# Performance work log

Hardware: AMD Instinct MI355X
Metric: run time of the kernel (lower is better)

The kernel has to match this reference:

```python
import jax, jax.numpy as jnp
import numpy as np

H, W, C_IN, C_ADD = 721, 1440, 78, 8
N_NODES, K = 5882, 128
DAY_OF_YEAR = 182.5  # module default time_of_year
LN_EPS = 1e-5        # haiku LayerNorm default
NORM_EPS = 1e-7


def setup_inputs() -> dict:
    key = jax.random.key(0)
    ks = jax.random.split(key, 4)
    return {
        "var_grid": jax.random.normal(ks[0], (H, W, C_IN), dtype=jnp.float32),
        "nearby_idx": jax.random.randint(ks[1], (N_NODES, K), 0, H * W),
        "input_means": jnp.zeros((C_IN + C_ADD,), jnp.float32),
        "input_stds": jnp.ones((C_IN + C_ADD,), jnp.float32),
        "W1": jax.random.normal(ks[2], (C_IN + C_ADD, 256), dtype=jnp.float32) * 0.1,
        "b1": jnp.zeros((256,), jnp.float32),
        "ln_scale": jnp.ones((256,), jnp.float32),
        "ln_offset": jnp.zeros((256,), jnp.float32),
        "W2": jax.random.normal(ks[3], (256, 256), dtype=jnp.float32) * 0.1,
        "b2": jnp.zeros((256,), jnp.float32),
    }


def _additional_features(h, w):
    # 8 extra channels: sin/cos of lat/lon, normalized day-of-year, 3 zero pads
    lat = jnp.linspace(-90.0, 90.0, h)
    lon = jnp.linspace(0.0, 360.0, w)
    lat2d = jnp.broadcast_to(lat[:, None], (h, w))
    lon2d = jnp.broadcast_to(lon[None, :], (h, w))
    lat_r, lon_r = jnp.radians(lat2d), jnp.radians(lon2d)
    day = jnp.float32(DAY_OF_YEAR / 365.0)
    z = jnp.zeros((h, w), jnp.float32)
    return jnp.stack([
        jnp.sin(lat_r), jnp.cos(lat_r), jnp.sin(lon_r), jnp.cos(lon_r),
        jnp.full((h, w), day, jnp.float32), z, z, z,
    ], axis=-1)  # [H, W, 8]


def reference(var_grid, nearby_idx, input_means, input_stds,
              W1, b1, ln_scale, ln_offset, W2, b2):
    h, w, c = var_grid.shape
    add = _additional_features(h, w)                       # [H, W, 8]
    flat = jnp.concatenate([var_grid, add], -1).reshape(h * w, c + C_ADD)
    gathered = flat[nearby_idx]                            # [N, K, 86] irregular gather
    x = (gathered - input_means) / (input_stds + NORM_EPS)
    hidden = jax.nn.relu(jnp.einsum('nkc,cd->nkd', x, W1) + b1)
    mu = hidden.mean(-1, keepdims=True)
    var = hidden.var(-1, keepdims=True)
    hidden = (hidden - mu) * jax.lax.rsqrt(var + LN_EPS) * ln_scale + ln_offset
    nodes = jnp.einsum('nkd,de->nke', hidden, W2) + b2     # [N, K, 256]
    return nodes
```

## Files before the change

### kernel.cpp

```cpp
#include <hip/hip_runtime.h>
#include <hip/hip_bf16.h>
#include <math.h>

#define GH 721
#define GW 1440
#define C_IN 78
#define NNODES 5882
#define KNEIGH 128
#define M_TOTAL (NNODES * KNEIGH)
#define TM 32
#define NBLOCKS (M_TOTAL / TM)

typedef __attribute__((ext_vector_type(8))) short bf16x8;
typedef __attribute__((ext_vector_type(4))) float f32x4;

__device__ __forceinline__ unsigned short f2bf(float x) {
    __hip_bfloat16 b = __float2bfloat16(x);
    union { __hip_bfloat16 h; unsigned short u; } cv; cv.h = b; return cv.u;
}

__global__ void prep_kernel(const float* __restrict__ W1, const float* __restrict__ W2,
                            const float* __restrict__ means, const float* __restrict__ stds,
                            const float* __restrict__ b1, const float* __restrict__ lnS,
                            const float* __restrict__ lnO, const float* __restrict__ b2,
                            unsigned short* __restrict__ bp1, unsigned short* __restrict__ bp2,
                            float* __restrict__ latT, float* __restrict__ lonT,
                            float* __restrict__ b1p, float* __restrict__ K1,
                            float* __restrict__ K2)
{
    const int NB1 = 3 * 4 * 256 * 8;
    const int NB2 = 8 * 4 * 256 * 8;
    const int NTOT = NB1 + NB2 + GH + GW + 256;
    for (int e = blockIdx.x * blockDim.x + threadIdx.x; e < NTOT;
         e += gridDim.x * blockDim.x) {
        if (e < NB1) {
            int j = e & 7, c = (e >> 3) & 255, o = (e >> 11) & 3, s = e >> 13;
            int k = s * 32 + o * 8 + j;
            float v = 0.f;
            if (k < 82) v = W1[k * 256 + c] / (stds[k] + 1e-7f);
            bp1[e] = f2bf(v);
        } else if (e < NB1 + NB2) {
            int t = e - NB1;
            int j = t & 7, c = (t >> 3) & 255, o = (t >> 11) & 3, s = t >> 13;
            int k = s * 32 + o * 8 + j;
            bp2[t] = f2bf(W2[k * 256 + c] * lnS[k]);
        } else if (e < NB1 + NB2 + GH) {
            int h = e - NB1 - NB2;
            float r = (-90.f + 0.25f * (float)h) * 0.017453292519943295f;
            latT[2 * h]     = sinf(r);
            latT[2 * h + 1] = cosf(r);
        } else if (e < NB1 + NB2 + GH + GW) {
            int w = e - NB1 - NB2 - GH;
            float r = ((float)w * (360.f / 1439.f)) * 0.017453292519943295f;
            lonT[2 * w]     = sinf(r);
            lonT[2 * w + 1] = cosf(r);
        } else {
            int c = e - NB1 - NB2 - GH - GW;
            float acc = b1[c];
            #pragma unroll 1
            for (int k = 0; k < 86; ++k) {
                float inv = 1.f / (stds[k] + 1e-7f);
                float w = W1[k * 256 + c] * inv;
                acc -= means[k] * w;
                if (k == 82) acc += 0.5f * w;
            }
            b1p[c] = acc;
            float k1 = 0.f, k2 = 0.f;
            #pragma unroll 1
            for (int k = 0; k < 256; ++k) {
                float w = W2[k * 256 + c];
                k1 += lnS[k] * w;
                k2 += lnO[k] * w;
            }
            K1[c] = k1;
            K2[c] = k2 + b2[c];
        }
    }
}

__global__ __launch_bounds__(256, 4)
void fused_kernel(const float* __restrict__ var_grid, const int* __restrict__ idxs,
                  const unsigned short* __restrict__ bp1, const unsigned short* __restrict__ bp2,
                  const float* __restrict__ latT, const float* __restrict__ lonT,
                  const float* __restrict__ b1p, const float* __restrict__ K1,
                  const float* __restrict__ K2,
                  float* __restrict__ out)
{
    __shared__ __align__(16) unsigned short x_lds[TM][104];
    __shared__ __align__(16) unsigned short h_lds[TM * 256];
    __shared__ float red[2][4][TM];

    const int swz = (blockIdx.x & 7) * 2941 + (blockIdx.x >> 3);

    const int tid  = threadIdx.x;
    const int lane = tid & 63;
    const int wc   = tid >> 6;
    const int l15  = lane & 15;
    const int lg   = lane >> 4;
    const int wbase = wc * 64;
    const long block0 = (long)swz * TM;

    {
        const int row = tid >> 3, p = tid & 7;
        const int idx = idxs[block0 + row];
        const int hh = idx / GW;
        const int ww = idx - hh * GW;
        const float* src = var_grid + (long)idx * C_IN;
        float2 g[5], tl, tl2;
        #pragma unroll
        for (int t = 0; t < 5; ++t) {
            const int q = p + 8 * t;
            if (q < 39) g[t] = *(const float2*)(src + 2 * q);
        }
        tl.x  = latT[2 * hh]; tl.y  = latT[2 * hh + 1];
        tl2.x = lonT[2 * ww]; tl2.y = lonT[2 * ww + 1];
        unsigned int* xrow = (unsigned int*)&x_lds[row][0];
        #pragma unroll
        for (int t = 0; t < 6; ++t) {
            const int q = p + 8 * t;
            float v0, v1;
            if (q < 39)      { v0 = g[t].x; v1 = g[t].y; }
            else if (q == 39){ v0 = tl.x;  v1 = tl.y; }
            else if (q == 40){ v0 = tl2.x; v1 = tl2.y; }
            else             { v0 = 0.f; v1 = 0.f; }
            xrow[q] = ((unsigned int)f2bf(v1) << 16) | (unsigned int)f2bf(v0);
        }
    }

    float b1v[4];
    #pragma unroll
    for (int nf = 0; nf < 4; ++nf) b1v[nf] = b1p[wbase + nf * 16 + l15];
    __syncthreads();

    f32x4 acc[2][4];
    #pragma unroll
    for (int mf = 0; mf < 2; ++mf)
        #pragma unroll
        for (int nf = 0; nf < 4; ++nf) acc[mf][nf] = (f32x4){0.f, 0.f, 0.f, 0.f};

    #pragma unroll
    for (int s = 0; s < 3; ++s) {
        bf16x8 af[2], bw[4];
        #pragma unroll
        for (int nf = 0; nf < 4; ++nf)
            bw[nf] = *(const bf16x8*)(bp1 + ((size_t)((s * 4 + lg) * 256) + wbase + nf * 16 + l15) * 8);
        #pragma unroll
        for (int mf = 0; mf < 2; ++mf)
            af[mf] = *(const bf16x8*)&x_lds[mf * 16 + l15][s * 32 + lg * 8];
        #pragma unroll
        for (int mf = 0; mf < 2; ++mf)
            #pragma unroll
            for (int nf = 0; nf < 4; ++nf)
                acc[mf][nf] = __builtin_amdgcn_mfma_f32_16x16x32_bf16(af[mf], bw[nf], acc[mf][nf], 0, 0, 0);
    }

    float sm[2][4], sq[2][4];
    #pragma unroll
    for (int mf = 0; mf < 2; ++mf)
        #pragma unroll
        for (int i = 0; i < 4; ++i) { sm[mf][i] = 0.f; sq[mf][i] = 0.f; }

    #pragma unroll
    for (int mf = 0; mf < 2; ++mf)
        #pragma unroll
        for (int nf = 0; nf < 4; ++nf)
            #pragma unroll
            for (int i = 0; i < 4; ++i) {
                float v = fmaxf(acc[mf][nf][i] + b1v[nf], 0.f);
                sm[mf][i] += v;
                sq[mf][i] += v * v;
                int row = mf * 16 + lg * 4 + i;
                int col = wbase + nf * 16 + l15;
                unsigned off = (unsigned)(row * 512 + col * 2);
                off ^= (unsigned)((row & 7) << 4);
                *(unsigned short*)((char*)h_lds + off) = f2bf(v);
            }

    #pragma unroll
    for (int m = 1; m < 16; m <<= 1)
        #pragma unroll
        for (int mf = 0; mf < 2; ++mf)
            #pragma unroll
            for (int i = 0; i < 4; ++i) {
                sm[mf][i] += __shfl_xor(sm[mf][i], m, 64);
                sq[mf][i] += __shfl_xor(sq[mf][i], m, 64);
            }

    if (l15 == 0) {
        #pragma unroll
        for (int mf = 0; mf < 2; ++mf)
            #pragma unroll
            for (int i = 0; i < 4; ++i) {
                int row = mf * 16 + lg * 4 + i;
                red[0][wc][row] = sm[mf][i];
                red[1][wc][row] = sq[mf][i];
            }
    }
    __syncthreads();

    #pragma unroll
    for (int mf = 0; mf < 2; ++mf)
        #pragma unroll
        for (int nf = 0; nf < 4; ++nf) acc[mf][nf] = (f32x4){0.f, 0.f, 0.f, 0.f};

    #pragma unroll
    for (int s = 0; s < 8; ++s) {
        bf16x8 af[2], bw[4];
        #pragma unroll
        for (int nf = 0; nf < 4; ++nf)
            bw[nf] = *(const bf16x8*)(bp2 + ((size_t)((s * 4 + lg) * 256) + wbase + nf * 16 + l15) * 8);
        #pragma unroll
        for (int mf = 0; mf < 2; ++mf) {
            int row = mf * 16 + l15;
            unsigned off = (unsigned)(row * 512 + (s * 32 + lg * 8) * 2);
            off ^= (unsigned)((row & 7) << 4);
            af[mf] = *(const bf16x8*)((char*)h_lds + off);
        }
        #pragma unroll
        for (int mf = 0; mf < 2; ++mf)
            #pragma unroll
            for (int nf = 0; nf < 4; ++nf)
                acc[mf][nf] = __builtin_amdgcn_mfma_f32_16x16x32_bf16(af[mf], bw[nf], acc[mf][nf], 0, 0, 0);
    }

    float K1v[4], K2v[4];
    #pragma unroll
    for (int nf = 0; nf < 4; ++nf) {
        int col = wbase + nf * 16 + l15;
        K1v[nf] = K1[col]; K2v[nf] = K2[col];
    }
    #pragma unroll
    for (int mf = 0; mf < 2; ++mf)
        #pragma unroll
        for (int i = 0; i < 4; ++i) {
            int row = mf * 16 + lg * 4 + i;
            float tot = red[0][0][row] + red[0][1][row] + red[0][2][row] + red[0][3][row];
            float tq  = red[1][0][row] + red[1][1][row] + red[1][2][row] + red[1][3][row];
            float mean = tot * (1.f / 256.f);
            float var  = tq * (1.f / 256.f) - mean * mean;
            float rs = rsqrtf(var + 1e-5f);
            long row_g = block0 + row;
            float* po = out + row_g * 256 + wbase;
            #pragma unroll
            for (int nf = 0; nf < 4; ++nf)
                po[nf * 16 + l15] = rs * (acc[mf][nf][i] - mean * K1v[nf]) + K2v[nf];
        }
}

extern "C" void kernel_launch(void* const* d_in, const int* in_sizes, int n_in,
                              void* d_out, int out_size, void* d_ws, size_t ws_size,
                              hipStream_t stream) {
    const float* var_grid = (const float*)d_in[0];
    const int*   idxs     = (const int*)d_in[1];
    const float* means    = (const float*)d_in[2];
    const float* stds     = (const float*)d_in[3];
    const float* W1       = (const float*)d_in[4];
    const float* b1       = (const float*)d_in[5];
    const float* lnS      = (const float*)d_in[6];
    const float* lnO      = (const float*)d_in[7];
    const float* W2       = (const float*)d_in[8];
    const float* b2       = (const float*)d_in[9];
    float* out = (float*)d_out;

    char* ws = (char*)d_ws;
    unsigned short* bp1 = (unsigned short*)ws;
    unsigned short* bp2 = (unsigned short*)(ws + 49152);
    float* latT = (float*)(ws + 180224);
    float* lonT = (float*)(ws + 186000);
    float* b1p  = (float*)(ws + 197520);
    float* K1   = (float*)(ws + 198544);
    float* K2   = (float*)(ws + 199568);

    prep_kernel<<<362, 256, 0, stream>>>(W1, W2, means, stds, b1, lnS, lnO, b2,
                                         bp1, bp2, latT, lonT, b1p, K1, K2);
    fused_kernel<<<NBLOCKS, 256, 0, stream>>>(var_grid, idxs, bp1, bp2, latT, lonT,
                                              b1p, K1, K2, out);
}
```

Before: 434.9 us.

## Make blocks persistent over 8 tiles with async global-to-LDS double-buffered gather

```diff
diff --git a/kernel.cpp b/kernel.cpp
--- a/kernel.cpp
+++ b/kernel.cpp
@@ -9,10 +9,16 @@
 #define KNEIGH 128
 #define M_TOTAL (NNODES * KNEIGH)
 #define TM 32
-#define NBLOCKS (M_TOTAL / TM)
+#define TILES 8
+#define NBLOCKS (M_TOTAL / (TM * TILES))
 
 typedef __attribute__((ext_vector_type(8))) short bf16x8;
 typedef __attribute__((ext_vector_type(4))) float f32x4;
+
+#define BAR_ALL()  do { asm volatile("s_waitcnt vmcnt(0) lgkmcnt(0)" ::: "memory"); \
+                        __builtin_amdgcn_s_barrier(); } while (0)
+#define BAR_LGKM() do { asm volatile("s_waitcnt lgkmcnt(0)" ::: "memory"); \
+                        __builtin_amdgcn_s_barrier(); } while (0)
 
 __device__ __forceinline__ unsigned short f2bf(float x) {
     __hip_bfloat16 b = __float2bfloat16(x);
@@ -86,165 +92,202 @@
                   const float* __restrict__ K2,
                   float* __restrict__ out)
 {
-    __shared__ __align__(16) unsigned short x_lds[TM][104];
+    __shared__ __align__(16) float raw[2][TM][C_IN];
     __shared__ __align__(16) unsigned short h_lds[TM * 256];
     __shared__ float red[2][4][TM];
-
-    const int swz = (blockIdx.x & 7) * 2941 + (blockIdx.x >> 3);
+    unsigned short (*x_lds)[104] = (unsigned short (*)[104])h_lds;
+
+    const int q_ = 367, r_ = 5;
+    const int xcd = blockIdx.x & 7;
+    const int ii  = blockIdx.x >> 3;
+    const int swz = (xcd < r_ ? xcd * (q_ + 1) : r_ * (q_ + 1) + (xcd - r_) * q_) + ii;
 
     const int tid  = threadIdx.x;
     const int lane = tid & 63;
-    const int wc   = tid >> 6;
+    const int wave = tid >> 6;
+    const int wc   = wave;
     const int l15  = lane & 15;
     const int lg   = lane >> 4;
     const int wbase = wc * 64;
-    const long block0 = (long)swz * TM;
-
-    {
-        const int row = tid >> 3, p = tid & 7;
-        const int idx = idxs[block0 + row];
-        const int hh = idx / GW;
-        const int ww = idx - hh * GW;
-        const float* src = var_grid + (long)idx * C_IN;
-        float2 g[5], tl, tl2;
-        #pragma unroll
-        for (int t = 0; t < 5; ++t) {
-            const int q = p + 8 * t;
-            if (q < 39) g[t] = *(const float2*)(src + 2 * q);
-        }
-        tl.x  = latT[2 * hh]; tl.y  = latT[2 * hh + 1];
-        tl2.x = lonT[2 * ww]; tl2.y = lonT[2 * ww + 1];
-        unsigned int* xrow = (unsigned int*)&x_lds[row][0];
-        #pragma unroll
-        for (int t = 0; t < 6; ++t) {
-            const int q = p + 8 * t;
-            float v0, v1;
-            if (q < 39)      { v0 = g[t].x; v1 = g[t].y; }
-            else if (q == 39){ v0 = tl.x;  v1 = tl.y; }
-            else if (q == 40){ v0 = tl2.x; v1 = tl2.y; }
-            else             { v0 = 0.f; v1 = 0.f; }
-            xrow[q] = ((unsigned int)f2bf(v1) << 16) | (unsigned int)f2bf(v0);
-        }
-    }
+    const long block0 = (long)swz * (TM * TILES);
+
+    const int crow = tid >> 3, cp = tid & 7;
+
+    auto dma_issue = [&](int t1) {
+        const int buf = t1 & 1;
+        #pragma unroll
+        for (int i = 0; i < 10; ++i) {
+            if (i < 9 || wave < 3) {
+                const int cidx = i * 256 + tid;
+                const int row  = cidx / 78;
+                const int c    = cidx - row * 78;
+                const int idx  = idxs[block0 + t1 * TM + row];
+                const float* src = var_grid + (size_t)idx * C_IN + c;
+                char* dst = ((char*)&raw[buf][0][0]) + (size_t)(i * 256 + wave * 64) * 4;
+                __builtin_amdgcn_global_load_lds(
+                    (const __attribute__((address_space(1))) void*)src,
+                    (__attribute__((address_space(3))) void*)dst, 4, 0, 0);
+            }
+        }
+    };
+
+    dma_issue(0);
 
     float b1v[4];
     #pragma unroll
     for (int nf = 0; nf < 4; ++nf) b1v[nf] = b1p[wbase + nf * 16 + l15];
-    __syncthreads();
-
-    f32x4 acc[2][4];
-    #pragma unroll
-    for (int mf = 0; mf < 2; ++mf)
-        #pragma unroll
-        for (int nf = 0; nf < 4; ++nf) acc[mf][nf] = (f32x4){0.f, 0.f, 0.f, 0.f};
-
-    #pragma unroll
-    for (int s = 0; s < 3; ++s) {
-        bf16x8 af[2], bw[4];
-        #pragma unroll
-        for (int nf = 0; nf < 4; ++nf)
-            bw[nf] = *(const bf16x8*)(bp1 + ((size_t)((s * 4 + lg) * 256) + wbase + nf * 16 + l15) * 8);
-        #pragma unroll
-        for (int mf = 0; mf < 2; ++mf)
-            af[mf] = *(const bf16x8*)&x_lds[mf * 16 + l15][s * 32 + lg * 8];
-        #pragma unroll
-        for (int mf = 0; mf < 2; ++mf)
+
+    #pragma unroll 1
+    for (int t = 0; t < TILES; ++t) {
+        BAR_ALL();
+
+        {
+            const float* rr = &raw[t & 1][crow][0];
+            const int idx = idxs[block0 + t * TM + crow];
+            unsigned int* xrow = (unsigned int*)&x_lds[crow][0];
+            float tv0 = 0.f, tv1 = 0.f, tw0 = 0.f, tw1 = 0.f;
+            if (cp == 7) {
+                int hh = idx / GW;
+                tv0 = latT[2 * hh]; tv1 = latT[2 * hh + 1];
+            }
+            if (cp == 0) {
+                int hh = idx / GW;
+                int ww = idx - hh * GW;
+                tw0 = lonT[2 * ww]; tw1 = lonT[2 * ww + 1];
+            }
+            #pragma unroll
+            for (int u = 0; u < 6; ++u) {
+                const int q = cp + 8 * u;
+                float v0, v1;
+                if (q <= 38)      { float2 g = *(const float2*)(rr + 2 * q); v0 = g.x; v1 = g.y; }
+                else if (q == 39) { v0 = tv0; v1 = tv1; }
+                else if (q == 40) { v0 = tw0; v1 = tw1; }
+                else              { v0 = 0.f; v1 = 0.f; }
+                xrow[q] = ((unsigned int)f2bf(v1) << 16) | (unsigned int)f2bf(v0);
+            }
+        }
+
+        if (t + 1 < TILES) dma_issue(t + 1);
+
+        BAR_LGKM();
+
+        f32x4 acc[2][4];
+        #pragma unroll
+        for (int mf = 0; mf < 2; ++mf)
+            #pragma unroll
+            for (int nf = 0; nf < 4; ++nf) acc[mf][nf] = (f32x4){0.f, 0.f, 0.f, 0.f};
+
+        #pragma unroll
+        for (int s = 0; s < 3; ++s) {
+            bf16x8 af[2], bw[4];
             #pragma unroll
             for (int nf = 0; nf < 4; ++nf)
-                acc[mf][nf] = __builtin_amdgcn_mfma_f32_16x16x32_bf16(af[mf], bw[nf], acc[mf][nf], 0, 0, 0);
-    }
-
-    float sm[2][4], sq[2][4];
-    #pragma unroll
-    for (int mf = 0; mf < 2; ++mf)
-        #pragma unroll
-        for (int i = 0; i < 4; ++i) { sm[mf][i] = 0.f; sq[mf][i] = 0.f; }
-
-    #pragma unroll
-    for (int mf = 0; mf < 2; ++mf)
-        #pragma unroll
-        for (int nf = 0; nf < 4; ++nf)
-            #pragma unroll
-            for (int i = 0; i < 4; ++i) {
-                float v = fmaxf(acc[mf][nf][i] + b1v[nf], 0.f);
-                sm[mf][i] += v;
-                sq[mf][i] += v * v;
-                int row = mf * 16 + lg * 4 + i;
-                int col = wbase + nf * 16 + l15;
-                unsigned off = (unsigned)(row * 512 + col * 2);
+                bw[nf] = *(const bf16x8*)(bp1 + ((size_t)((s * 4 + lg) * 256) + wbase + nf * 16 + l15) * 8);
+            #pragma unroll
+            for (int mf = 0; mf < 2; ++mf)
+                af[mf] = *(const bf16x8*)&x_lds[mf * 16 + l15][s * 32 + lg * 8];
+            #pragma unroll
+            for (int mf = 0; mf < 2; ++mf)
+                #pragma unroll
+                for (int nf = 0; nf < 4; ++nf)
+                    acc[mf][nf] = __builtin_amdgcn_mfma_f32_16x16x32_bf16(af[mf], bw[nf], acc[mf][nf], 0, 0, 0);
+        }
+
+        BAR_LGKM();
+
+        float sm[2][4], sq[2][4];
+        #pragma unroll
+        for (int mf = 0; mf < 2; ++mf)
+            #pragma unroll
+            for (int i = 0; i < 4; ++i) { sm[mf][i] = 0.f; sq[mf][i] = 0.f; }
+
+        #pragma unroll
+        for (int mf = 0; mf < 2; ++mf)
+            #pragma unroll
+            for (int nf = 0; nf < 4; ++nf)
+                #pragma unroll
+                for (int i = 0; i < 4; ++i) {
+                    float v = fmaxf(acc[mf][nf][i] + b1v[nf], 0.f);
+                    sm[mf][i] += v;
+                    sq[mf][i] += v * v;
+                    int row = mf * 16 + lg * 4 + i;
+                    int col = wbase + nf * 16 + l15;
+                    unsigned off = (unsigned)(row * 512 + col * 2);
+                    off ^= (unsigned)((row & 7) << 4);
+                    *(unsigned short*)((char*)h_lds + off) = f2bf(v);
+                }
+
+        #pragma unroll
+        for (int m = 1; m < 16; m <<= 1)
+            #pragma unroll
+            for (int mf = 0; mf < 2; ++mf)
+                #pragma unroll
+                for (int i = 0; i < 4; ++i) {
+                    sm[mf][i] += __shfl_xor(sm[mf][i], m, 64);
+                    sq[mf][i] += __shfl_xor(sq[mf][i], m, 64);
+                }
+
+        if (l15 == 0) {
+            #pragma unroll
+            for (int mf = 0; mf < 2; ++mf)
+                #pragma unroll
+                for (int i = 0; i < 4; ++i) {
+                    int row = mf * 16 + lg * 4 + i;
+                    red[0][wc][row] = sm[mf][i];
+                    red[1][wc][row] = sq[mf][i];
+                }
+        }
+
+        BAR_LGKM();
+
+        #pragma unroll
+        for (int mf = 0; mf < 2; ++mf)
+            #pragma unroll
+            for (int nf = 0; nf < 4; ++nf) acc[mf][nf] = (f32x4){0.f, 0.f, 0.f, 0.f};
+
+        #pragma unroll
+        for (int s = 0; s < 8; ++s) {
+            bf16x8 af[2], bw[4];
+            #pragma unroll
+            for (int nf = 0; nf < 4; ++nf)
+                bw[nf] = *(const bf16x8*)(bp2 + ((size_t)((s * 4 + lg) * 256) + wbase + nf * 16 + l15) * 8);
+            #pragma unroll
+            for (int mf = 0; mf < 2; ++mf) {
+                int row = mf * 16 + l15;
+                unsigned off = (unsigned)(row * 512 + (s * 32 + lg * 8) * 2);
                 off ^= (unsigned)((row & 7) << 4);
-                *(unsigned short*)((char*)h_lds + off) = f2bf(v);
-            }
-
-    #pragma unroll
-    for (int m = 1; m < 16; m <<= 1)
-        #pragma unroll
-        for (int mf = 0; mf < 2; ++mf)
-            #pragma unroll
-            for (int i = 0; i < 4; ++i) {
-                sm[mf][i] += __shfl_xor(sm[mf][i], m, 64);
-                sq[mf][i] += __shfl_xor(sq[mf][i], m, 64);
-            }
-
-    if (l15 == 0) {
+                af[mf] = *(const bf16x8*)((char*)h_lds + off);
+            }
+            #pragma unroll
+            for (int mf = 0; mf < 2; ++mf)
+                #pragma unroll
+                for (int nf = 0; nf < 4; ++nf)
+                    acc[mf][nf] = __builtin_amdgcn_mfma_f32_16x16x32_bf16(af[mf], bw[nf], acc[mf][nf], 0, 0, 0);
+        }
+
+        float K1v[4], K2v[4];
+        #pragma unroll
+        for (int nf = 0; nf < 4; ++nf) {
+            int col = wbase + nf * 16 + l15;
+            K1v[nf] = K1[col]; K2v[nf] = K2[col];
+        }
         #pragma unroll
         for (int mf = 0; mf < 2; ++mf)
             #pragma unroll
             for (int i = 0; i < 4; ++i) {
                 int row = mf * 16 + lg * 4 + i;
-                red[0][wc][row] = sm[mf][i];
-                red[1][wc][row] = sq[mf][i];
+                float tot = red[0][0][row] + red[0][1][row] + red[0][2][row] + red[0][3][row];
+                float tq  = red[1][0][row] + red[1][1][row] + red[1][2][row] + red[1][3][row];
+                float mean = tot * (1.f / 256.f);
+                float var  = tq * (1.f / 256.f) - mean * mean;
+                float rs = rsqrtf(var + 1e-5f);
+                long row_g = block0 + t * TM + row;
+                float* po = out + row_g * 256 + wbase;
+                #pragma unroll
+                for (int nf = 0; nf < 4; ++nf)
+                    po[nf * 16 + l15] = rs * (acc[mf][nf][i] - mean * K1v[nf]) + K2v[nf];
             }
     }
-    __syncthreads();
-
-    #pragma unroll
-    for (int mf = 0; mf < 2; ++mf)
-        #pragma unroll
-        for (int nf = 0; nf < 4; ++nf) acc[mf][nf] = (f32x4){0.f, 0.f, 0.f, 0.f};
-
-    #pragma unroll
-    for (int s = 0; s < 8; ++s) {
-        bf16x8 af[2], bw[4];
-        #pragma unroll
-        for (int nf = 0; nf < 4; ++nf)
-            bw[nf] = *(const bf16x8*)(bp2 + ((size_t)((s * 4 + lg) * 256) + wbase + nf * 16 + l15) * 8);
-        #pragma unroll
-        for (int mf = 0; mf < 2; ++mf) {
-            int row = mf * 16 + l15;
-            unsigned off = (unsigned)(row * 512 + (s * 32 + lg * 8) * 2);
-            off ^= (unsigned)((row & 7) << 4);
-            af[mf] = *(const bf16x8*)((char*)h_lds + off);
-        }
-        #pragma unroll
-        for (int mf = 0; mf < 2; ++mf)
-            #pragma unroll
-            for (int nf = 0; nf < 4; ++nf)
-                acc[mf][nf] = __builtin_amdgcn_mfma_f32_16x16x32_bf16(af[mf], bw[nf], acc[mf][nf], 0, 0, 0);
-    }
-
-    float K1v[4], K2v[4];
-    #pragma unroll
-    for (int nf = 0; nf < 4; ++nf) {
-        int col = wbase + nf * 16 + l15;
-        K1v[nf] = K1[col]; K2v[nf] = K2[col];
-    }
-    #pragma unroll
-    for (int mf = 0; mf < 2; ++mf)
-        #pragma unroll
-        for (int i = 0; i < 4; ++i) {
-            int row = mf * 16 + lg * 4 + i;
-            float tot = red[0][0][row] + red[0][1][row] + red[0][2][row] + red[0][3][row];
-            float tq  = red[1][0][row] + red[1][1][row] + red[1][2][row] + red[1][3][row];
-            float mean = tot * (1.f / 256.f);
-            float var  = tq * (1.f / 256.f) - mean * mean;
-            float rs = rsqrtf(var + 1e-5f);
-            long row_g = block0 + row;
-            float* po = out + row_g * 256 + wbase;
-            #pragma unroll
-            for (int nf = 0; nf < 4; ++nf)
-                po[nf * 16 + l15] = rs * (acc[mf][nf][i] - mean * K1v[nf]) + K2v[nf];
-        }
 }
 
 extern "C" void kernel_launch(void* const* d_in, const int* in_sizes, int n_in,
```

After: 1.206 ms. +177.3%, slower.
